# Performance work log

Measured on AMD Instinct MI355X. Metric: run time of the kernel, lower is better.

The kernel has to match this reference:

```python
import jax, jax.numpy as jnp
import numpy as np

H = 64
N_NODES = 12000
N_EDGES = 50000


def setup_inputs() -> dict:
    key = jax.random.key(0)
    ks = jax.random.split(key, 16)
    s = 1.0 / np.sqrt(H)
    inp = {
        "node": jax.random.normal(ks[0], (N_NODES, H), jnp.float32),
        "edge": jax.random.normal(ks[1], (N_EDGES, H), jnp.float32),
        "hidden_feats": jax.random.normal(ks[2], (N_NODES, H), jnp.float32),
        "src": jax.random.randint(ks[3], (N_EDGES,), 0, N_NODES, jnp.int32),
        "dst": jax.random.randint(ks[4], (N_EDGES,), 0, N_NODES, jnp.int32),
        # edge_network: Linear(H, 2H) -> ReLU -> Linear(2H, H*H)
        "W1": jax.random.uniform(ks[5], (2 * H, H), jnp.float32, -s, s),
        "b1": jax.random.uniform(ks[6], (2 * H,), jnp.float32, -s, s),
        "W2": jax.random.uniform(ks[7], (H * H, 2 * H), jnp.float32, -1 / np.sqrt(2 * H), 1 / np.sqrt(2 * H)),
        "b2": jax.random.uniform(ks[8], (H * H,), jnp.float32, -1 / np.sqrt(2 * H), 1 / np.sqrt(2 * H)),
        # GRUCell params (torch layout: [3H, H], gate order r,z,n)
        "W_ih": jax.random.uniform(ks[9], (3 * H, H), jnp.float32, -s, s),
        "W_hh": jax.random.uniform(ks[10], (3 * H, H), jnp.float32, -s, s),
        "b_ih": jax.random.uniform(ks[11], (3 * H,), jnp.float32, -s, s),
        "b_hh": jax.random.uniform(ks[12], (3 * H,), jnp.float32, -s, s),
        # LayerNorm params
        "gamma": jnp.ones((H,), jnp.float32),
        "beta": jnp.zeros((H,), jnp.float32),
    }
    return inp


def _gru_cell(x, h, W_ih, W_hh, b_ih, b_hh):
    gi = x @ W_ih.T + b_ih  # [N, 3H]
    gh = h @ W_hh.T + b_hh  # [N, 3H]
    r = jax.nn.sigmoid(gi[:, :H] + gh[:, :H])
    z = jax.nn.sigmoid(gi[:, H:2 * H] + gh[:, H:2 * H])
    n = jnp.tanh(gi[:, 2 * H:] + r * gh[:, 2 * H:])
    return (1.0 - z) * n + z * h


def reference(node, edge, hidden_feats, src, dst, W1, b1, W2, b2,
              W_ih, W_hh, b_ih, b_hh, gamma, beta):
    n_nodes = node.shape[0]
    # edge network -> per-edge [H,H] weight matrices
    eh = jax.nn.relu(edge @ W1.T + b1)                      # [E, 2H]
    Wedge = (eh @ W2.T + b2).reshape(-1, H, H)              # [E, H, H]
    # gather src feats, per-edge matmul (row-vector @ matrix), scatter-sum to dst
    msg = jnp.einsum('eh,ehk->ek', node[src], Wedge)        # [E, H]
    agg = jax.ops.segment_sum(msg, dst, num_segments=n_nodes)  # [N, H]
    new_node_feats = jax.nn.relu(agg)
    out = _gru_cell(new_node_feats, hidden_feats, W_ih, W_hh, b_ih, b_hh)
    # LayerNorm (eps=1e-5)
    mu = jnp.mean(out, axis=-1, keepdims=True)
    var = jnp.var(out, axis=-1, keepdims=True)
    out = (out - mu) * jax.lax.rsqrt(var + 1e-5) * gamma + beta
    return out
```

## Files before the change

kernel.cpp:

```cpp
#include <hip/hip_runtime.h>

#define H 64
#define NEDGE 50000
#define NNODE 12000
#define EPAD 50176

typedef _Float16 f16;
typedef _Float16 h8 __attribute__((ext_vector_type(8)));
typedef float f4 __attribute__((ext_vector_type(4)));

#define O_EDGEH 0ull
#define O_W2G   6422528ull
#define O_W1G   7471104ull
#define O_WG    7487488ull
#define O_NB    7553024ull
#define O_AGG   10625024ull

__device__ __forceinline__ void async16(const void* g, void* l) {
  __builtin_amdgcn_global_load_lds((const __attribute__((address_space(1))) void*)g,
                                   (__attribute__((address_space(3))) void*)l, 16, 0, 0);
}

__global__ __launch_bounds__(256) void k_prep(const float* __restrict__ edge, const float* __restrict__ W1,
                                              const float* __restrict__ W2, const float* __restrict__ b2,
                                              const float* __restrict__ node,
                                              const float* __restrict__ Wih, const float* __restrict__ Whh,
                                              f16* __restrict__ edgeh, f16* __restrict__ w1g, f16* __restrict__ w2g,
                                              f16* __restrict__ wg, float* __restrict__ nb, float* __restrict__ agg) {
  int bid = blockIdx.x;
  int t = threadIdx.x;
  if (bid < 750) {
    int id = bid * 256 + t;
    *(f4*)(agg + (long)id * 4) = (f4){0.f, 0.f, 0.f, 0.f};
    return;
  }
  if (bid < 2318) {
    long id8 = (long)(bid - 750) * 256 + t;
    long e = id8 >> 3;
    int c = (int)(id8 & 7) * 8;
    h8 o = {};
    if (e < NEDGE) {
      const float* p = edge + e * 64 + c;
      f4 v0 = *(const f4*)p, v1 = *(const f4*)(p + 4);
#pragma unroll
      for (int j = 0; j < 4; ++j) { o[j] = (f16)v0[j]; o[4 + j] = (f16)v1[j]; }
    }
    *(h8*)(edgeh + e * 64 + c) = o;
    return;
  }
  if (bid < 4366) {
    int id = (bid - 2318) * 256 + t;
    int ii = id & 7, l = (id >> 3) & 63, t4 = (id >> 9) & 3, s = (id >> 11) & 3, h = id >> 13;
    int n = t4 * 16 + (l & 15), j = s * 32 + ((l >> 4) << 3) + ii;
    w2g[id] = (f16)W2[(h * 64 + n) * 128 + j];
    return;
  }
  if (bid < 4398) {
    int id = (bid - 4366) * 256 + t;
    int ii = id & 7, l = (id >> 3) & 63, tt = (id >> 9) & 7, s = id >> 12;
    int n = tt * 16 + (l & 15), k = s * 32 + ((l >> 4) << 3) + ii;
    w1g[id] = (f16)W1[n * 64 + k];
    return;
  }
  if (bid < 4526) {
    int id = (bid - 4398) * 256 + t;
    int ii = id & 7, l = (id >> 3) & 63, tt = (id >> 9) & 15, s = id >> 13;
    int k = s * 32 + ((l >> 4) << 3) + ii, n = tt * 16 + (l & 15);
    float v;
    if (n < 128) v = (k < 64) ? Wih[n * 64 + k] : Whh[n * 64 + (k - 64)];
    else if (n < 192) v = (k < 64) ? Wih[n * 64 + k] : 0.f;
    else v = (k < 64) ? 0.f : Whh[(n - 64) * 64 + (k - 64)];
    wg[id] = (f16)v;
    return;
  }
  __shared__ float bs[64][65];
  __shared__ float xs[64][65];
  int n0 = (bid - 4526) * 64;
#pragma unroll
  for (int it = 0; it < 16; ++it) {
    int idx = t + it * 256;
    int rr = idx >> 6, cc = idx & 63;
    bs[rr][cc] = b2[idx];
    int nn = n0 + rr;
    xs[rr][cc] = (nn < NNODE) ? node[(long)nn * 64 + cc] : 0.f;
  }
  __syncthreads();
  int f0 = (t & 15) * 4, e0 = (t >> 4) * 4;
  float acc[4][4] = {};
#pragma unroll 4
  for (int k = 0; k < 64; ++k) {
    f4 w = *(const f4*)&bs[k][f0];
#pragma unroll
    for (int i = 0; i < 4; ++i) {
      float x = xs[e0 + i][k];
      acc[i][0] = fmaf(x, w[0], acc[i][0]); acc[i][1] = fmaf(x, w[1], acc[i][1]);
      acc[i][2] = fmaf(x, w[2], acc[i][2]); acc[i][3] = fmaf(x, w[3], acc[i][3]);
    }
  }
#pragma unroll
  for (int i = 0; i < 4; ++i) {
    int nn = n0 + e0 + i;
    if (nn < NNODE)
#pragma unroll
      for (int j = 0; j < 4; ++j) nb[(long)nn * 64 + f0 + j] = acc[i][j];
  }
}

__global__ __launch_bounds__(256, 2) void k_msg(const float* __restrict__ node,
                                                const int* __restrict__ src, const int* __restrict__ dst,
                                                const f16* __restrict__ edgeh, const f16* __restrict__ w1g,
                                                const f16* __restrict__ w2g, const float* __restrict__ b1,
                                                const float* __restrict__ nbt, float* __restrict__ agg) {
  __shared__ __align__(16) char lds[104960];
  f16* eh_s = (f16*)lds;
  char* bbuf = lds;
  int* ssrc = (int*)(lds + 102400);
  int* sdst = (int*)(lds + 103424);
  float* b1s = (float*)(lds + 104448);

  int t = threadIdx.x;
  int e_base = blockIdx.x * 256;

  {
    int eg = e_base + t;
    bool valid = eg < NEDGE;
    int si = valid ? src[eg] : 0;
    ssrc[t] = si;
    sdst[t] = valid ? dst[eg] : 0;
    if (t < 128) b1s[t] = b1[t];
    const f4* nr = (const f4*)(node + (long)si * 64);
    f16* vrow = (f16*)(lds + 65536 + t * 144);
#pragma unroll
    for (int b = 0; b < 8; ++b) {
      f4 v0 = nr[b * 2], v1 = nr[b * 2 + 1];
      h8 pk;
#pragma unroll
      for (int m = 0; m < 4; ++m) { pk[m] = (f16)v0[m]; pk[4 + m] = (f16)v1[m]; }
      *(h8*)(vrow + b * 8) = pk;
    }
  }
  __syncthreads();

  int wave = t >> 6, lane = t & 63;
  int l15 = lane & 15, lq = lane >> 4;
  int ew0 = wave * 64;

  {
    h8 afr[4][2];
#pragma unroll
    for (int g = 0; g < 4; ++g)
#pragma unroll
      for (int s = 0; s < 2; ++s)
        afr[g][s] = *(const h8*)(edgeh + (long)(e_base + ew0 + g * 16 + l15) * 64 + s * 32 + lq * 8);
#pragma unroll
    for (int nh = 0; nh < 2; ++nh) {
      h8 bfr[2][4];
#pragma unroll
      for (int s = 0; s < 2; ++s)
#pragma unroll
        for (int tt = 0; tt < 4; ++tt)
          bfr[s][tt] = *(const h8*)(w1g + ((s * 8 + nh * 4 + tt) * 64 + lane) * 8);
      f4 acc_eh[4][4];
#pragma unroll
      for (int g = 0; g < 4; ++g)
#pragma unroll
        for (int tt = 0; tt < 4; ++tt) acc_eh[g][tt] = (f4){0.f, 0.f, 0.f, 0.f};
#pragma unroll
      for (int s = 0; s < 2; ++s)
#pragma unroll
        for (int g = 0; g < 4; ++g)
#pragma unroll
          for (int tt = 0; tt < 4; ++tt)
            acc_eh[g][tt] = __builtin_amdgcn_mfma_f32_16x16x32_f16(afr[g][s], bfr[s][tt], acc_eh[g][tt], 0, 0, 0);
#pragma unroll
      for (int g = 0; g < 4; ++g)
#pragma unroll
        for (int tt = 0; tt < 4; ++tt) {
          int n = (nh * 4 + tt) * 16 + l15;
          int jg = n >> 3;
#pragma unroll
          for (int r = 0; r < 4; ++r) {
            int e = ew0 + g * 16 + lq * 4 + r;
            float val = fmaxf(acc_eh[g][tt][r] + b1s[n], 0.f);
            eh_s[(e * 16 + (jg ^ (e & 15))) * 8 + (n & 7)] = (f16)val;
          }
        }
    }
  }
  __syncthreads();

  h8 ehreg[4][4];
#pragma unroll
  for (int g = 0; g < 4; ++g) {
    int e = ew0 + g * 16 + l15;
#pragma unroll
    for (int s = 0; s < 4; ++s)
      ehreg[g][s] = *(const h8*)(eh_s + (e * 16 + ((s * 4 + lq) ^ (e & 15))) * 8);
  }
  __syncthreads();

  const char* w2b = (const char*)w2g;
#pragma unroll
  for (int r = 0; r < 8; ++r) async16(w2b + r * 4096 + t * 16, bbuf + r * 4096 + t * 16);

  f4 acc[4][4];
#pragma unroll
  for (int g = 0; g < 4; ++g)
#pragma unroll
    for (int tt = 0; tt < 4; ++tt) acc[g][tt] = (f4){0.f, 0.f, 0.f, 0.f};

#pragma unroll 1
  for (int hpb = 0; hpb < 8; ++hpb) {
    h8 vh8[4];
#pragma unroll
    for (int g = 0; g < 4; ++g)
      vh8[g] = *(const h8*)(lds + 65536 + (ew0 + g * 16 + l15) * 144 + hpb * 16);
#pragma unroll
    for (int hpi = 0; hpi < 4; ++hpi) {
      int hp = hpb * 4 + hpi;
      __syncthreads();
      {
        const char* gsrc = w2b + (long)(hp + 1) * 32768;
        char* ldst = bbuf + ((hp + 1) & 1) * 32768;
#pragma unroll
        for (int r = 0; r < 8; ++r) async16(gsrc + r * 4096 + t * 16, ldst + r * 4096 + t * 16);
      }
      const char* bp = bbuf + (hp & 1) * 32768;
#pragma unroll
      for (int sub = 0; sub < 2; ++sub) {
        const f16* bc = (const f16*)(bp + sub * 16384);
        const int hh = hpi * 2 + sub;
#pragma unroll
        for (int s = 0; s < 4; ++s) {
          h8 bf[4];
#pragma unroll
          for (int tt = 0; tt < 4; ++tt)
            bf[tt] = *(const h8*)(bc + ((s * 4 + tt) * 64 + lane) * 8);
#pragma unroll
          for (int g = 0; g < 4; ++g) {
            h8 a = ehreg[g][s] * vh8[g][hh];
#pragma unroll
            for (int tt = 0; tt < 4; ++tt)
              acc[g][tt] = __builtin_amdgcn_mfma_f32_16x16x32_f16(a, bf[tt], acc[g][tt], 0, 0, 0);
          }
        }
      }
    }
  }

#pragma unroll
  for (int g = 0; g < 4; ++g)
#pragma unroll
    for (int tt = 0; tt < 4; ++tt)
#pragma unroll
      for (int r = 0; r < 4; ++r) {
        int el = ew0 + g * 16 + lq * 4 + r;
        if (e_base + el < NEDGE) {
          int n = tt * 16 + l15;
          float v = acc[g][tt][r] + nbt[(long)ssrc[el] * 64 + n];
          atomicAdd(&agg[(long)sdst[el] * 64 + n], v);
        }
      }
}

__global__ __launch_bounds__(256) void k_node(const float* __restrict__ agg, const float* __restrict__ hid,
                                              const f16* __restrict__ wg,
                                              const float* __restrict__ bih, const float* __restrict__ bhh,
                                              const float* __restrict__ gamma, const float* __restrict__ beta,
                                              float* __restrict__ out) {
  __shared__ __align__(16) f16 xh_s[128 * 136];
  __shared__ float bsum[128], bin_s[64], bhn_s[64], gam_s[64], bet_s[64];
  int t = threadIdx.x;
  int n0 = blockIdx.x * 128;

  if (t < 128) bsum[t] = bih[t] + bhh[t];
  else if (t < 192) bin_s[t - 128] = bih[t];
  else bhn_s[t - 192] = bhh[t - 64];
  if (t < 64) gam_s[t] = gamma[t];
  else if (t < 128) bet_s[t - 64] = beta[t - 64];

  {
    int m = t >> 1, half = t & 1;
    int mg = n0 + m;
    bool vld = mg < NNODE;
    const float* sp = half ? (hid + (long)mg * 64) : (agg + (long)mg * 64);
#pragma unroll
    for (int jj = 0; jj < 8; ++jj) {
      f4 v0 = {0, 0, 0, 0}, v1 = {0, 0, 0, 0};
      if (vld) { v0 = *(const f4*)(sp + jj * 8); v1 = *(const f4*)(sp + jj * 8 + 4); }
      h8 pk;
#pragma unroll
      for (int m2 = 0; m2 < 4; ++m2) {
        pk[m2] = (f16)(half ? v0[m2] : fmaxf(v0[m2], 0.f));
        pk[4 + m2] = (f16)(half ? v1[m2] : fmaxf(v1[m2], 0.f));
      }
      *(h8*)(xh_s + m * 136 + half * 64 + jj * 8) = pk;
    }
  }
  __syncthreads();

  int wave = t >> 6, lane = t & 63;
  int l15 = lane & 15, lq = lane >> 4;

  f4 acc[2][16];
#pragma unroll
  for (int g = 0; g < 2; ++g)
#pragma unroll
    for (int tt = 0; tt < 16; ++tt) acc[g][tt] = (f4){0.f, 0.f, 0.f, 0.f};

#pragma unroll
  for (int s = 0; s < 4; ++s) {
    h8 a0 = *(const h8*)(xh_s + (wave * 32 + l15) * 136 + s * 32 + lq * 8);
    h8 a1 = *(const h8*)(xh_s + (wave * 32 + 16 + l15) * 136 + s * 32 + lq * 8);
#pragma unroll
    for (int tt = 0; tt < 16; ++tt) {
      h8 b = *(const h8*)(wg + ((s * 16 + tt) * 64 + lane) * 8);
      acc[0][tt] = __builtin_amdgcn_mfma_f32_16x16x32_f16(a0, b, acc[0][tt], 0, 0, 0);
      acc[1][tt] = __builtin_amdgcn_mfma_f32_16x16x32_f16(a1, b, acc[1][tt], 0, 0, 0);
    }
  }

#pragma unroll
  for (int g = 0; g < 2; ++g)
#pragma unroll
    for (int r = 0; r < 4; ++r) {
      int mg = n0 + wave * 32 + g * 16 + lq * 4 + r;
      bool vld = mg < NNODE;
      float o[4], ssum = 0.f, s2 = 0.f;
#pragma unroll
      for (int t0 = 0; t0 < 4; ++t0) {
        int f = t0 * 16 + l15;
        float rpre = acc[g][t0][r] + bsum[f];
        float zpre = acc[g][4 + t0][r] + bsum[64 + f];
        float ginv = acc[g][8 + t0][r] + bin_s[f];
        float ghnv = acc[g][12 + t0][r] + bhn_s[f];
        float rr = 1.f / (1.f + __expf(-rpre));
        float zz = 1.f / (1.f + __expf(-zpre));
        float hv = vld ? hid[(long)mg * 64 + f] : 0.f;
        float nn = tanhf(ginv + rr * ghnv);
        float oo = (1.f - zz) * nn + zz * hv;
        o[t0] = oo; ssum += oo; s2 += oo * oo;
      }
#pragma unroll
      for (int d = 1; d < 16; d <<= 1) {
        ssum += __shfl_xor(ssum, d);
        s2 += __shfl_xor(s2, d);
      }
      float mu = ssum * (1.f / 64.f);
      float var = s2 * (1.f / 64.f) - mu * mu;
      float rstd = rsqrtf(var + 1e-5f);
      if (vld)
#pragma unroll
        for (int t0 = 0; t0 < 4; ++t0) {
          int f = t0 * 16 + l15;
          out[(long)mg * 64 + f] = (o[t0] - mu) * rstd * gam_s[f] + bet_s[f];
        }
    }
}

extern "C" void kernel_launch(void* const* d_in, const int* in_sizes, int n_in,
                              void* d_out, int out_size, void* d_ws, size_t ws_size,
                              hipStream_t stream) {
  const float* node = (const float*)d_in[0];
  const float* edge = (const float*)d_in[1];
  const float* hid = (const float*)d_in[2];
  const int* src = (const int*)d_in[3];
  const int* dst = (const int*)d_in[4];
  const float* W1 = (const float*)d_in[5];
  const float* b1 = (const float*)d_in[6];
  const float* W2 = (const float*)d_in[7];
  const float* b2 = (const float*)d_in[8];
  const float* Wih = (const float*)d_in[9];
  const float* Whh = (const float*)d_in[10];
  const float* bih = (const float*)d_in[11];
  const float* bhh = (const float*)d_in[12];
  const float* gamma = (const float*)d_in[13];
  const float* beta = (const float*)d_in[14];

  char* ws = (char*)d_ws;
  f16* edgeh = (f16*)(ws + O_EDGEH);
  f16* w2g = (f16*)(ws + O_W2G);
  f16* w1g = (f16*)(ws + O_W1G);
  f16* wg = (f16*)(ws + O_WG);
  float* nb = (float*)(ws + O_NB);
  float* agg = (float*)(ws + O_AGG);

  k_prep<<<4714, 256, 0, stream>>>(edge, W1, W2, b2, node, Wih, Whh, edgeh, w1g, w2g, wg, nb, agg);
  k_msg<<<196, 256, 0, stream>>>(node, src, dst, edgeh, w1g, w2g, b1, nb, agg);
  k_node<<<94, 256, 0, stream>>>(agg, hid, wg, bih, bhh, gamma, beta, (float*)d_out);
}
```

Measured before the change: 214.2 us.

## Retile message kernel with 32x32 MFMA, smaller blocks, and folded b2 bias

The message kernel now handles 128 edges per block with 32x32x16 MFMA tiles, doubling the grid and roughly halving LDS so three blocks can share a CU. The b2 bias term is no longer a separate node-level precompute. It is stored in fp16 right after the W2 tiles and applied as an extra K-step in the same MFMA loop, so the final prefetch lands on it naturally. This removes the nb workspace and the per-edge gather of it in the epilogue, and makes better use of CUs that the old 196-block grid left idle. In exchange, the bias is now multiplied in fp16 rather than fp32, and each block streams all of W2 for fewer edges, which raises total W2 traffic.

```diff
diff --git a/kernel.cpp b/kernel.cpp
--- a/kernel.cpp
+++ b/kernel.cpp
@@ -8,25 +8,32 @@
 typedef _Float16 f16;
 typedef _Float16 h8 __attribute__((ext_vector_type(8)));
 typedef float f4 __attribute__((ext_vector_type(4)));
+typedef float fv16 __attribute__((ext_vector_type(16)));
 
 #define O_EDGEH 0ull
 #define O_W2G   6422528ull
-#define O_W1G   7471104ull
-#define O_WG    7487488ull
-#define O_NB    7553024ull
-#define O_AGG   10625024ull
+#define O_B2G   7471104ull
+#define O_W1G   7479296ull
+#define O_WG    7495680ull
+#define O_AGG   7561216ull
 
 __device__ __forceinline__ void async16(const void* g, void* l) {
   __builtin_amdgcn_global_load_lds((const __attribute__((address_space(1))) void*)g,
                                    (__attribute__((address_space(3))) void*)l, 16, 0, 0);
 }
 
+__device__ __forceinline__ fv16 zero16() {
+  fv16 z;
+#pragma unroll
+  for (int i = 0; i < 16; ++i) z[i] = 0.f;
+  return z;
+}
+
 __global__ __launch_bounds__(256) void k_prep(const float* __restrict__ edge, const float* __restrict__ W1,
                                               const float* __restrict__ W2, const float* __restrict__ b2,
-                                              const float* __restrict__ node,
                                               const float* __restrict__ Wih, const float* __restrict__ Whh,
                                               f16* __restrict__ edgeh, f16* __restrict__ w1g, f16* __restrict__ w2g,
-                                              f16* __restrict__ wg, float* __restrict__ nb, float* __restrict__ agg) {
+                                              f16* __restrict__ b2g, f16* __restrict__ wg, float* __restrict__ agg) {
   int bid = blockIdx.x;
   int t = threadIdx.x;
   if (bid < 750) {
@@ -50,20 +57,27 @@
   }
   if (bid < 4366) {
     int id = (bid - 2318) * 256 + t;
-    int ii = id & 7, l = (id >> 3) & 63, t4 = (id >> 9) & 3, s = (id >> 11) & 3, h = id >> 13;
-    int n = t4 * 16 + (l & 15), j = s * 32 + ((l >> 4) << 3) + ii;
+    int i = id & 7, l = (id >> 3) & 63, nh = (id >> 9) & 1, s = (id >> 10) & 7, h = id >> 13;
+    int n = nh * 32 + (l & 31), j = s * 16 + ((l >> 5) << 3) + i;
     w2g[id] = (f16)W2[(h * 64 + n) * 128 + j];
     return;
   }
-  if (bid < 4398) {
+  if (bid < 4382) {
     int id = (bid - 4366) * 256 + t;
-    int ii = id & 7, l = (id >> 3) & 63, tt = (id >> 9) & 7, s = id >> 12;
-    int n = tt * 16 + (l & 15), k = s * 32 + ((l >> 4) << 3) + ii;
+    int i = id & 7, l = (id >> 3) & 63, nh = (id >> 9) & 1, s = id >> 10;
+    int n = nh * 32 + (l & 31), k = s * 16 + ((l >> 5) << 3) + i;
+    b2g[id] = (f16)b2[k * 64 + n];
+    return;
+  }
+  if (bid < 4414) {
+    int id = (bid - 4382) * 256 + t;
+    int i = id & 7, l = (id >> 3) & 63, nt = (id >> 9) & 3, s = id >> 11;
+    int n = nt * 32 + (l & 31), k = s * 16 + ((l >> 5) << 3) + i;
     w1g[id] = (f16)W1[n * 64 + k];
     return;
   }
-  if (bid < 4526) {
-    int id = (bid - 4398) * 256 + t;
+  {
+    int id = (bid - 4414) * 256 + t;
     int ii = id & 7, l = (id >> 3) & 63, tt = (id >> 9) & 15, s = id >> 13;
     int k = s * 32 + ((l >> 4) << 3) + ii, n = tt * 16 + (l & 15);
     float v;
@@ -71,196 +85,163 @@
     else if (n < 192) v = (k < 64) ? Wih[n * 64 + k] : 0.f;
     else v = (k < 64) ? 0.f : Whh[(n - 64) * 64 + (k - 64)];
     wg[id] = (f16)v;
-    return;
-  }
-  __shared__ float bs[64][65];
-  __shared__ float xs[64][65];
-  int n0 = (bid - 4526) * 64;
-#pragma unroll
-  for (int it = 0; it < 16; ++it) {
-    int idx = t + it * 256;
-    int rr = idx >> 6, cc = idx & 63;
-    bs[rr][cc] = b2[idx];
-    int nn = n0 + rr;
-    xs[rr][cc] = (nn < NNODE) ? node[(long)nn * 64 + cc] : 0.f;
-  }
-  __syncthreads();
-  int f0 = (t & 15) * 4, e0 = (t >> 4) * 4;
-  float acc[4][4] = {};
-#pragma unroll 4
-  for (int k = 0; k < 64; ++k) {
-    f4 w = *(const f4*)&bs[k][f0];
-#pragma unroll
-    for (int i = 0; i < 4; ++i) {
-      float x = xs[e0 + i][k];
-      acc[i][0] = fmaf(x, w[0], acc[i][0]); acc[i][1] = fmaf(x, w[1], acc[i][1]);
-      acc[i][2] = fmaf(x, w[2], acc[i][2]); acc[i][3] = fmaf(x, w[3], acc[i][3]);
-    }
-  }
-#pragma unroll
-  for (int i = 0; i < 4; ++i) {
-    int nn = n0 + e0 + i;
-    if (nn < NNODE)
-#pragma unroll
-      for (int j = 0; j < 4; ++j) nb[(long)nn * 64 + f0 + j] = acc[i][j];
-  }
-}
-
-__global__ __launch_bounds__(256, 2) void k_msg(const float* __restrict__ node,
+  }
+}
+
+__global__ __launch_bounds__(256, 3) void k_msg(const float* __restrict__ node,
                                                 const int* __restrict__ src, const int* __restrict__ dst,
                                                 const f16* __restrict__ edgeh, const f16* __restrict__ w1g,
                                                 const f16* __restrict__ w2g, const float* __restrict__ b1,
-                                                const float* __restrict__ nbt, float* __restrict__ agg) {
-  __shared__ __align__(16) char lds[104960];
+                                                float* __restrict__ agg) {
+  __shared__ __align__(16) char lds[52736];
   f16* eh_s = (f16*)lds;
   char* bbuf = lds;
-  int* ssrc = (int*)(lds + 102400);
-  int* sdst = (int*)(lds + 103424);
-  float* b1s = (float*)(lds + 104448);
+  f16* vT = (f16*)(lds + 32768);
+  int* ssrc = (int*)(lds + 51200);
+  int* sdst = (int*)(lds + 51712);
+  float* b1s = (float*)(lds + 52224);
 
   int t = threadIdx.x;
-  int e_base = blockIdx.x * 256;
-
-  {
+  int e_base = blockIdx.x * 128;
+
+  if (t < 128) {
     int eg = e_base + t;
     bool valid = eg < NEDGE;
-    int si = valid ? src[eg] : 0;
-    ssrc[t] = si;
+    ssrc[t] = valid ? src[eg] : 0;
     sdst[t] = valid ? dst[eg] : 0;
-    if (t < 128) b1s[t] = b1[t];
-    const f4* nr = (const f4*)(node + (long)si * 64);
-    f16* vrow = (f16*)(lds + 65536 + t * 144);
-#pragma unroll
-    for (int b = 0; b < 8; ++b) {
+  } else {
+    b1s[t - 128] = b1[t - 128];
+  }
+  {
+    int e = t >> 1, half = t & 1;
+    int eg = e_base + e;
+    int si = (eg < NEDGE) ? src[eg] : 0;
+    const f4* nr = (const f4*)(node + (long)si * 64 + half * 32);
+#pragma unroll
+    for (int b = 0; b < 4; ++b) {
       f4 v0 = nr[b * 2], v1 = nr[b * 2 + 1];
       h8 pk;
 #pragma unroll
       for (int m = 0; m < 4; ++m) { pk[m] = (f16)v0[m]; pk[4 + m] = (f16)v1[m]; }
-      *(h8*)(vrow + b * 8) = pk;
+      *(h8*)(vT + e * 72 + (half * 4 + b) * 8) = pk;
     }
   }
   __syncthreads();
 
   int wave = t >> 6, lane = t & 63;
-  int l15 = lane & 15, lq = lane >> 4;
-  int ew0 = wave * 64;
-
-  {
-    h8 afr[4][2];
-#pragma unroll
-    for (int g = 0; g < 4; ++g)
-#pragma unroll
-      for (int s = 0; s < 2; ++s)
-        afr[g][s] = *(const h8*)(edgeh + (long)(e_base + ew0 + g * 16 + l15) * 64 + s * 32 + lq * 8);
-#pragma unroll
-    for (int nh = 0; nh < 2; ++nh) {
-      h8 bfr[2][4];
-#pragma unroll
-      for (int s = 0; s < 2; ++s)
-#pragma unroll
-        for (int tt = 0; tt < 4; ++tt)
-          bfr[s][tt] = *(const h8*)(w1g + ((s * 8 + nh * 4 + tt) * 64 + lane) * 8);
-      f4 acc_eh[4][4];
-#pragma unroll
-      for (int g = 0; g < 4; ++g)
-#pragma unroll
-        for (int tt = 0; tt < 4; ++tt) acc_eh[g][tt] = (f4){0.f, 0.f, 0.f, 0.f};
-#pragma unroll
-      for (int s = 0; s < 2; ++s)
-#pragma unroll
-        for (int g = 0; g < 4; ++g)
-#pragma unroll
-          for (int tt = 0; tt < 4; ++tt)
-            acc_eh[g][tt] = __builtin_amdgcn_mfma_f32_16x16x32_f16(afr[g][s], bfr[s][tt], acc_eh[g][tt], 0, 0, 0);
-#pragma unroll
-      for (int g = 0; g < 4; ++g)
-#pragma unroll
-        for (int tt = 0; tt < 4; ++tt) {
-          int n = (nh * 4 + tt) * 16 + l15;
-          int jg = n >> 3;
-#pragma unroll
-          for (int r = 0; r < 4; ++r) {
-            int e = ew0 + g * 16 + lq * 4 + r;
-            float val = fmaxf(acc_eh[g][tt][r] + b1s[n], 0.f);
-            eh_s[(e * 16 + (jg ^ (e & 15))) * 8 + (n & 7)] = (f16)val;
-          }
+  int wm = wave & 1, wn = wave >> 1;
+  int l31 = lane & 31, lh = lane >> 5;
+
+  {
+    h8 afr[2][4];
+#pragma unroll
+    for (int mt = 0; mt < 2; ++mt)
+#pragma unroll
+      for (int s = 0; s < 4; ++s)
+        afr[mt][s] = *(const h8*)(edgeh + (long)(e_base + wm * 64 + mt * 32 + l31) * 64 + s * 16 + lh * 8);
+    h8 bfr[2][4];
+#pragma unroll
+    for (int nt = 0; nt < 2; ++nt)
+#pragma unroll
+      for (int s = 0; s < 4; ++s)
+        bfr[nt][s] = *(const h8*)(w1g + ((s * 4 + wn * 2 + nt) * 64 + lane) * 8);
+    fv16 acc_eh[2][2];
+#pragma unroll
+    for (int mt = 0; mt < 2; ++mt)
+#pragma unroll
+      for (int nt = 0; nt < 2; ++nt) acc_eh[mt][nt] = zero16();
+#pragma unroll
+    for (int s = 0; s < 4; ++s)
+#pragma unroll
+      for (int mt = 0; mt < 2; ++mt)
+#pragma unroll
+        for (int nt = 0; nt < 2; ++nt)
+          acc_eh[mt][nt] = __builtin_amdgcn_mfma_f32_32x32x16_f16(afr[mt][s], bfr[nt][s], acc_eh[mt][nt], 0, 0, 0);
+#pragma unroll
+    for (int mt = 0; mt < 2; ++mt)
+#pragma unroll
+      for (int nt = 0; nt < 2; ++nt)
+#pragma unroll
+        for (int r = 0; r < 16; ++r) {
+          int row = (r & 3) + 8 * (r >> 2) + 4 * lh;
+          int e = wm * 64 + mt * 32 + row;
+          int n = wn * 64 + nt * 32 + l31;
+          float val = fmaxf(acc_eh[mt][nt][r] + b1s[n], 0.f);
+          int o = n >> 3;
+          eh_s[e * 128 + ((o ^ (e & 15)) << 3) + (n & 7)] = (f16)val;
         }
-    }
-  }
-  __syncthreads();
-
-  h8 ehreg[4][4];
-#pragma unroll
-  for (int g = 0; g < 4; ++g) {
-    int e = ew0 + g * 16 + l15;
-#pragma unroll
-    for (int s = 0; s < 4; ++s)
-      ehreg[g][s] = *(const h8*)(eh_s + (e * 16 + ((s * 4 + lq) ^ (e & 15))) * 8);
+  }
+  __syncthreads();
+
+  h8 ehreg[2][8];
+#pragma unroll
+  for (int mt = 0; mt < 2; ++mt) {
+    int e = wm * 64 + mt * 32 + l31;
+#pragma unroll
+    for (int s = 0; s < 8; ++s) {
+      int o = (s * 2 + lh) ^ (e & 15);
+      ehreg[mt][s] = *(const h8*)(eh_s + e * 128 + o * 8);
+    }
   }
   __syncthreads();
 
   const char* w2b = (const char*)w2g;
 #pragma unroll
-  for (int r = 0; r < 8; ++r) async16(w2b + r * 4096 + t * 16, bbuf + r * 4096 + t * 16);
-
-  f4 acc[4][4];
-#pragma unroll
-  for (int g = 0; g < 4; ++g)
-#pragma unroll
-    for (int tt = 0; tt < 4; ++tt) acc[g][tt] = (f4){0.f, 0.f, 0.f, 0.f};
+  for (int r = 0; r < 4; ++r) async16(w2b + r * 4096 + t * 16, bbuf + r * 4096 + t * 16);
+
+  fv16 acc[2];
+  acc[0] = zero16(); acc[1] = zero16();
+  const f16* vrow0 = vT + (wm * 64 + l31) * 72;
+  const f16* vrow1 = vT + (wm * 64 + 32 + l31) * 72;
 
 #pragma unroll 1
-  for (int hpb = 0; hpb < 8; ++hpb) {
-    h8 vh8[4];
-#pragma unroll
-    for (int g = 0; g < 4; ++g)
-      vh8[g] = *(const h8*)(lds + 65536 + (ew0 + g * 16 + l15) * 144 + hpb * 16);
-#pragma unroll
-    for (int hpi = 0; hpi < 4; ++hpi) {
-      int hp = hpb * 4 + hpi;
+  for (int hb = 0; hb < 8; ++hb) {
+    h8 vh0 = *(const h8*)(vrow0 + hb * 8);
+    h8 vh1 = *(const h8*)(vrow1 + hb * 8);
+#pragma unroll
+    for (int hh = 0; hh < 8; ++hh) {
+      int h = hb * 8 + hh;
       __syncthreads();
       {
-        const char* gsrc = w2b + (long)(hp + 1) * 32768;
-        char* ldst = bbuf + ((hp + 1) & 1) * 32768;
-#pragma unroll
-        for (int r = 0; r < 8; ++r) async16(gsrc + r * 4096 + t * 16, ldst + r * 4096 + t * 16);
-      }
-      const char* bp = bbuf + (hp & 1) * 32768;
-#pragma unroll
-      for (int sub = 0; sub < 2; ++sub) {
-        const f16* bc = (const f16*)(bp + sub * 16384);
-        const int hh = hpi * 2 + sub;
-#pragma unroll
-        for (int s = 0; s < 4; ++s) {
-          h8 bf[4];
-#pragma unroll
-          for (int tt = 0; tt < 4; ++tt)
-            bf[tt] = *(const h8*)(bc + ((s * 4 + tt) * 64 + lane) * 8);
-#pragma unroll
-          for (int g = 0; g < 4; ++g) {
-            h8 a = ehreg[g][s] * vh8[g][hh];
-#pragma unroll
-            for (int tt = 0; tt < 4; ++tt)
-              acc[g][tt] = __builtin_amdgcn_mfma_f32_16x16x32_f16(a, bf[tt], acc[g][tt], 0, 0, 0);
-          }
-        }
-      }
-    }
-  }
-
-#pragma unroll
-  for (int g = 0; g < 4; ++g)
-#pragma unroll
-    for (int tt = 0; tt < 4; ++tt)
-#pragma unroll
-      for (int r = 0; r < 4; ++r) {
-        int el = ew0 + g * 16 + lq * 4 + r;
-        if (e_base + el < NEDGE) {
-          int n = tt * 16 + l15;
-          float v = acc[g][tt][r] + nbt[(long)ssrc[el] * 64 + n];
-          atomicAdd(&agg[(long)sdst[el] * 64 + n], v);
-        }
-      }
+        const char* gsrc = w2b + (long)(h + 1) * 16384;
+        char* ldst = bbuf + ((h + 1) & 1) * 16384;
+#pragma unroll
+        for (int r = 0; r < 4; ++r) async16(gsrc + r * 4096 + t * 16, ldst + r * 4096 + t * 16);
+      }
+      const f16* bp = (const f16*)(bbuf + (h & 1) * 16384) + (wn * 64 + lane) * 8;
+      f16 v0 = vh0[hh], v1 = vh1[hh];
+#pragma unroll
+      for (int s = 0; s < 8; ++s) {
+        h8 bf = *(const h8*)(bp + s * 1024);
+        h8 a0 = ehreg[0][s] * v0;
+        acc[0] = __builtin_amdgcn_mfma_f32_32x32x16_f16(a0, bf, acc[0], 0, 0, 0);
+        h8 a1 = ehreg[1][s] * v1;
+        acc[1] = __builtin_amdgcn_mfma_f32_32x32x16_f16(a1, bf, acc[1], 0, 0, 0);
+      }
+    }
+  }
+  __syncthreads();
+  {
+    const f16* bp = (const f16*)bbuf + (wn * 64 + lane) * 8;
+#pragma unroll
+    for (int s = 0; s < 4; ++s) {
+      h8 bf = *(const h8*)(bp + s * 1024);
+      h8 a0 = *(const h8*)(vrow0 + (s * 2 + lh) * 8);
+      h8 a1 = *(const h8*)(vrow1 + (s * 2 + lh) * 8);
+      acc[0] = __builtin_amdgcn_mfma_f32_32x32x16_f16(a0, bf, acc[0], 0, 0, 0);
+      acc[1] = __builtin_amdgcn_mfma_f32_32x32x16_f16(a1, bf, acc[1], 0, 0, 0);
+    }
+  }
+
+  int n = wn * 32 + l31;
+#pragma unroll
+  for (int mt = 0; mt < 2; ++mt)
+#pragma unroll
+    for (int r = 0; r < 16; ++r) {
+      int el = wm * 64 + mt * 32 + (r & 3) + 8 * (r >> 2) + 4 * lh;
+      if (e_base + el < NEDGE)
+        atomicAdd(&agg[(long)sdst[el] * 64 + n], acc[mt][r]);
+    }
 }
 
 __global__ __launch_bounds__(256) void k_node(const float* __restrict__ agg, const float* __restrict__ hid,
@@ -380,12 +361,12 @@
   char* ws = (char*)d_ws;
   f16* edgeh = (f16*)(ws + O_EDGEH);
   f16* w2g = (f16*)(ws + O_W2G);
+  f16* b2g = (f16*)(ws + O_B2G);
   f16* w1g = (f16*)(ws + O_W1G);
   f16* wg = (f16*)(ws + O_WG);
-  float* nb = (float*)(ws + O_NB);
   float* agg = (float*)(ws + O_AGG);
 
-  k_prep<<<4714, 256, 0, stream>>>(edge, W1, W2, b2, node, Wih, Whh, edgeh, w1g, w2g, wg, nb, agg);
-  k_msg<<<196, 256, 0, stream>>>(node, src, dst, edgeh, w1g, w2g, b1, nb, agg);
+  k_prep<<<4542, 256, 0, stream>>>(edge, W1, W2, b2, Wih, Whh, edgeh, w1g, w2g, b2g, wg, agg);
+  k_msg<<<392, 256, 0, stream>>>(node, src, dst, edgeh, w1g, w2g, b1, agg);
   k_node<<<94, 256, 0, stream>>>(agg, hid, wg, bih, bhh, gamma, beta, (float*)d_out);
 }
```

New measurement: 186.5 us. -12.9%, faster.
